# Kernel tuning notes

Measured on AMD Instinct MI355X. Metric: run time of the kernel, lower is better.

Reference implementation:

```python
import jax, jax.numpy as jnp
import numpy as np

N_NODES = 50000
N_EDGES = 800000
D_FEAT = 128
EMBED = 128
HEADS = 8
HEAD_DIM = EMBED // HEADS


def setup_inputs() -> dict:
    key = jax.random.key(0)
    ks = jax.random.split(key, 10)
    xavier = jax.nn.initializers.xavier_normal()
    return {
        "nodes": jax.random.normal(ks[0], (N_NODES, D_FEAT), jnp.float32),
        "edges": jax.random.normal(ks[1], (N_EDGES, D_FEAT), jnp.float32),
        "senders": jax.random.randint(ks[2], (N_EDGES,), 0, N_NODES, jnp.int32),
        "receivers": jax.random.randint(ks[3], (N_EDGES,), 0, N_NODES, jnp.int32),
        "Ws_k": xavier(ks[4], (D_FEAT, EMBED), jnp.float32),
        "Ws_b": jnp.zeros((EMBED,), jnp.float32),
        "Wr_k": xavier(ks[5], (D_FEAT, EMBED), jnp.float32),
        "Wr_b": jnp.zeros((EMBED,), jnp.float32),
        "We_k": xavier(ks[6], (D_FEAT, EMBED), jnp.float32),
        "We_b": jnp.zeros((EMBED,), jnp.float32),
        "a": xavier(ks[7], (HEADS, HEAD_DIM), jnp.float32),
    }


def reference(nodes, edges, senders, receivers, Ws_k, Ws_b, Wr_k, Wr_b, We_k, We_b, a):
    N = nodes.shape[0]
    E = edges.shape[0]
    H, D = a.shape
    # Node-level projections (linear, so equivalent to projecting gathered edge endpoints)
    hs = nodes @ Ws_k + Ws_b            # [N, HD]  (W_s on sent attributes)
    hr = nodes @ Wr_k + Wr_b            # [N, HD]  (W_r on received attributes)
    he = edges @ We_k + We_b            # [E, HD]  (W_e on edge attributes)
    sent = hs[senders]                  # [E, HD]
    x = jax.nn.leaky_relu(sent + hr[receivers] + he)  # default slope 0.01, as original
    xh = x.reshape(E, H, D)
    logits = jnp.sum(xh * a, axis=-1)   # [E, H]
    # segment_softmax over receivers (stable: subtract per-segment max)
    mx = jax.ops.segment_max(logits, receivers, num_segments=N)  # [N, H]
    mx = jnp.where(jnp.isfinite(mx), mx, 0.0)
    ex = jnp.exp(logits - mx[receivers])                         # [E, H]
    denom = jax.ops.segment_sum(ex, receivers, num_segments=N)   # [N, H]
    w = ex / denom[receivers]                                    # [E, H]
    msg = (w[..., None] * sent.reshape(E, H, D)).reshape(E, H * D)
    out = jax.ops.segment_sum(msg, receivers, num_segments=N)    # [N, HD]
    return out
```

## Files before the change

### kernel.cpp

```cpp
#include <hip/hip_runtime.h>

#define N_NODES 50000
#define N_EDGES 800000
#define D 128
#define HEADS 8

typedef __attribute__((ext_vector_type(8))) short short8b;
typedef __attribute__((ext_vector_type(4))) float f32x4;

__device__ __forceinline__ unsigned short f2bf_rne(float f) {
    unsigned int u = __float_as_uint(f);
    u += 0x7FFFu + ((u >> 16) & 1u);
    return (unsigned short)(u >> 16);
}
__device__ __forceinline__ float bf2f(unsigned short u) {
    return __uint_as_float(((unsigned int)u) << 16);
}

template <int CTRL>
__device__ __forceinline__ float dpp_radd(float v) {
    int s = __builtin_amdgcn_update_dpp(0, __float_as_int(v), CTRL, 0xF, 0xF, true);
    return v + __int_as_float(s);
}
__device__ __forceinline__ float rowsum16(float v) {
    v = dpp_radd<0xB1>(v);
    v = dpp_radd<0x4E>(v);
    v = dpp_radd<0x141>(v);
    v = dpp_radd<0x140>(v);
    return v;
}

#define K1_ROWS 128
__global__ __launch_bounds__(256, 3) void k_node_proj_mfma(
    const float* __restrict__ nodes,
    const float* __restrict__ Ws, const float* __restrict__ bs,
    const float* __restrict__ Wr, const float* __restrict__ br,
    unsigned short* __restrict__ hsb, unsigned short* __restrict__ hrb)
{
    __shared__ __align__(16) unsigned short WT[D][136];
    __shared__ __align__(16) unsigned short At[64][136];
    const int ntiles = (N_NODES + K1_ROWS - 1) / K1_ROWS;
    int bx = blockIdx.x;
    int proj = (bx >= ntiles) ? 1 : 0;
    int tile = proj ? (bx - ntiles) : bx;
    const float* W    = proj ? Wr : Ws;
    const float* bias = proj ? br : bs;
    unsigned short* outp = proj ? hrb : hsb;
    int t = threadIdx.x;
    int lane = t & 63;
    int wv = t >> 6;
    int lg = lane >> 4;
    int li = lane & 15;

    #pragma unroll 8
    for (int j = 0; j < 64; ++j) {
        int idx = t + 256 * j;
        int k = idx >> 7, c = idx & 127;
        WT[c][k] = f2bf_rne(W[idx]);
    }
    float b_ct[8];
    #pragma unroll
    for (int ct = 0; ct < 8; ++ct) b_ct[ct] = bias[ct * 16 + li];

    #pragma unroll 1
    for (int sub = 0; sub < 2; ++sub) {
        int row0 = tile * K1_ROWS + sub * 64;
        if (row0 >= N_NODES) break;
        __syncthreads();
        {
            const float4* Nv = (const float4*)nodes;
            #pragma unroll
            for (int j = 0; j < 8; ++j) {
                int fi = t + 256 * j;
                int r = row0 + (fi >> 5);
                float4 v = make_float4(0.f, 0.f, 0.f, 0.f);
                if (r < N_NODES) v = Nv[(size_t)r * 32 + (fi & 31)];
                ushort4 b;
                b.x = f2bf_rne(v.x); b.y = f2bf_rne(v.y);
                b.z = f2bf_rne(v.z); b.w = f2bf_rne(v.w);
                *(ushort4*)&At[fi >> 5][(fi & 31) * 4] = b;
            }
        }
        __syncthreads();

        short8b afr[4];
        #pragma unroll
        for (int kb = 0; kb < 4; ++kb)
            afr[kb] = *(const short8b*)&At[wv * 16 + li][kb * 32 + lg * 8];

        #pragma unroll
        for (int ct = 0; ct < 8; ++ct) {
            f32x4 acc = {0.f, 0.f, 0.f, 0.f};
            #pragma unroll
            for (int kb = 0; kb < 4; ++kb) {
                short8b bfr = *(const short8b*)&WT[ct * 16 + li][kb * 32 + lg * 8];
                acc = __builtin_amdgcn_mfma_f32_16x16x32_bf16(afr[kb], bfr, acc, 0, 0, 0);
            }
            #pragma unroll
            for (int j = 0; j < 4; ++j) {
                int r = row0 + wv * 16 + lg * 4 + j;
                if (r < N_NODES)
                    outp[(size_t)r * D + ct * 16 + li] = f2bf_rne(acc[j] + b_ct[ct]);
            }
        }
    }
}

__global__ __launch_bounds__(256) void k_hist(
    const int* __restrict__ receivers, int* __restrict__ deg)
{
    int i = blockIdx.x * 256 + threadIdx.x;
    if (i < N_EDGES) atomicAdd(&deg[receivers[i]], 1);
}

#define SCAN_CHUNK 49
__global__ __launch_bounds__(1024) void k_scan(
    const int* __restrict__ deg, int* __restrict__ rowptr, int* __restrict__ cursor)
{
    __shared__ int sm[1024];
    int t = threadIdx.x;
    int base = t * SCAN_CHUNK;
    int lsum = 0;
    #pragma unroll 4
    for (int i = 0; i < SCAN_CHUNK; ++i) {
        int idx = base + i;
        if (idx < N_NODES) lsum += deg[idx];
    }
    sm[t] = lsum;
    __syncthreads();
    for (int off = 1; off < 1024; off <<= 1) {
        int v = (t >= off) ? sm[t - off] : 0;
        __syncthreads();
        sm[t] += v;
        __syncthreads();
    }
    int run = (t > 0) ? sm[t - 1] : 0;
    for (int i = 0; i < SCAN_CHUNK; ++i) {
        int idx = base + i;
        if (idx < N_NODES) {
            rowptr[idx] = run;
            cursor[idx] = run;
            run += deg[idx];
        }
    }
    if (t == 1023) rowptr[N_NODES] = sm[1023];
}

__global__ __launch_bounds__(256) void k_fill(
    const int* __restrict__ receivers, const int* __restrict__ senders,
    int* __restrict__ cursor,
    int* __restrict__ s_csr, int* __restrict__ pos_csr)
{
    int i = blockIdx.x * 256 + threadIdx.x;
    if (i < N_EDGES) {
        int r = receivers[i];
        int pos = atomicAdd(&cursor[r], 1);
        s_csr[pos]  = senders[i];
        pos_csr[i]  = pos;
    }
}

#define BLK_E 64
__global__ __launch_bounds__(256, 3) void k_edge_logits_mfma(
    const float* __restrict__ edges,
    const int* __restrict__ senders, const int* __restrict__ receivers,
    const int* __restrict__ pos_csr,
    const float* __restrict__ We, const float* __restrict__ be,
    const float* __restrict__ a,
    const unsigned short* __restrict__ hsb, const unsigned short* __restrict__ hrb,
    float* __restrict__ ex)
{
    __shared__ __align__(16) unsigned short WeT[D][136];
    __shared__ __align__(16) unsigned short Et[BLK_E][136];
    int t = threadIdx.x;
    int lane = t & 63;
    int wv = t >> 6;
    int lg = lane >> 4;
    int li = lane & 15;

    #pragma unroll 8
    for (int j = 0; j < 64; ++j) {
        int idx = t + 256 * j;
        int k = idx >> 7, c = idx & 127;
        WeT[c][k] = f2bf_rne(We[idx]);
    }
    float a_h[HEADS], be_h[HEADS];
    #pragma unroll
    for (int h = 0; h < HEADS; ++h) {
        a_h[h]  = a[h * 16 + li];
        be_h[h] = be[h * 16 + li];
    }
    __syncthreads();

    const int ntiles = N_EDGES / BLK_E;
    const float4* Ev = (const float4*)edges;

    for (int tile = blockIdx.x; tile < ntiles; tile += gridDim.x) {
        int pb = tile * BLK_E + wv * 16;

        #pragma unroll
        for (int j = 0; j < 8; ++j) {
            int fi = lane + 64 * j;
            int rloc = fi >> 5;
            float4 v = Ev[(size_t)(pb + rloc) * 32 + (fi & 31)];
            ushort4 b;
            b.x = f2bf_rne(v.x); b.y = f2bf_rne(v.y);
            b.z = f2bf_rne(v.z); b.w = f2bf_rne(v.w);
            *(ushort4*)&Et[wv * 16 + rloc][(fi & 31) * 4] = b;
        }

        int sj[4], rj[4];
        #pragma unroll
        for (int j = 0; j < 4; ++j) {
            sj[j] = senders[pb + lg * 4 + j];
            rj[j] = receivers[pb + lg * 4 + j];
        }
        int o = 4 * lg + (li >> 2);
        int mypos = pos_csr[pb + o];

        unsigned short g_hs[4][HEADS], g_hr[4][HEADS];
        #pragma unroll
        for (int j = 0; j < 4; ++j) {
            const unsigned short* hsrow = hsb + (size_t)sj[j] * D + li;
            const unsigned short* hrrow = hrb + (size_t)rj[j] * D + li;
            #pragma unroll
            for (int h = 0; h < HEADS; ++h) {
                g_hs[j][h] = hsrow[h * 16];
                g_hr[j][h] = hrrow[h * 16];
            }
        }

        asm volatile("s_waitcnt lgkmcnt(0)" ::: "memory");
        __builtin_amdgcn_sched_barrier(0);

        short8b afr[4];
        #pragma unroll
        for (int kb = 0; kb < 4; ++kb)
            afr[kb] = *(const short8b*)&Et[wv * 16 + li][kb * 32 + lg * 8];

        float hold[8];
        #pragma unroll
        for (int h = 0; h < HEADS; ++h) {
            f32x4 acc = {0.f, 0.f, 0.f, 0.f};
            #pragma unroll
            for (int kb = 0; kb < 4; ++kb) {
                short8b bfr = *(const short8b*)&WeT[h * 16 + li][kb * 32 + lg * 8];
                acc = __builtin_amdgcn_mfma_f32_16x16x32_bf16(afr[kb], bfr, acc, 0, 0, 0);
            }
            float pr[4];
            #pragma unroll
            for (int j = 0; j < 4; ++j) {
                float x = acc[j] + be_h[h] + bf2f(g_hs[j][h]) + bf2f(g_hr[j][h]);
                x = fmaxf(x, 0.01f * x);
                pr[j] = rowsum16(x * a_h[h]);
            }
            float qa = (li & 4) ? pr[1] : pr[0];
            float qb = (li & 4) ? pr[3] : pr[2];
            hold[h] = __expf((li & 8) ? qb : qa);
        }
        {
            float a0 = (li & 1) ? hold[2] : hold[0];
            float a1 = (li & 1) ? hold[6] : hold[4];
            float ea = (li & 2) ? a1 : a0;
            float b0 = (li & 1) ? hold[3] : hold[1];
            float b1 = (li & 1) ? hold[7] : hold[5];
            float eb = (li & 2) ? b1 : b0;
            int h1 = 2 * (li & 3);
            *(float2*)&ex[(size_t)mypos * HEADS + h1] = make_float2(ea, eb);
        }
        __builtin_amdgcn_wave_barrier();
    }
}

__global__ __launch_bounds__(256) void k_gather_out(
    const int* __restrict__ rowptr, const int* __restrict__ s_csr,
    const unsigned short* __restrict__ hsb, const float* __restrict__ ex,
    float* __restrict__ out)
{
    int r = blockIdx.x * 4 + (threadIdx.x >> 6);
    int l = threadIdx.x & 63;
    int h = l >> 3;
    int beg = rowptr[r], end = rowptr[r + 1];

    float2 acc = make_float2(0.f, 0.f);
    float dsum = 0.f;
    for (int j0 = beg; j0 < end; j0 += 16) {
        int cnt = end - j0;
        int s[16]; float w[16];
        #pragma unroll
        for (int q = 0; q < 16; ++q)
            if (q < cnt) { s[q] = s_csr[j0 + q]; w[q] = ex[(size_t)(j0 + q) * HEADS + h]; }
        #pragma unroll
        for (int q = 0; q < 16; ++q)
            if (q < cnt) {
                ushort2 hv = *(const ushort2*)&hsb[(size_t)s[q] * D + 2 * l];
                acc.x += w[q] * bf2f(hv.x);
                acc.y += w[q] * bf2f(hv.y);
                dsum  += w[q];
            }
    }
    float inv = (end > beg && dsum != 0.f) ? (1.0f / dsum) : 0.f;
    acc.x *= inv; acc.y *= inv;
    *(float2*)&out[(size_t)r * D + 2 * l] = acc;
}

extern "C" void kernel_launch(void* const* d_in, const int* in_sizes, int n_in,
                              void* d_out, int out_size, void* d_ws, size_t ws_size,
                              hipStream_t stream) {
    const float* nodes     = (const float*)d_in[0];
    const float* edges     = (const float*)d_in[1];
    const int*   senders   = (const int*)d_in[2];
    const int*   receivers = (const int*)d_in[3];
    const float* Ws = (const float*)d_in[4];
    const float* bs = (const float*)d_in[5];
    const float* Wr = (const float*)d_in[6];
    const float* br = (const float*)d_in[7];
    const float* We = (const float*)d_in[8];
    const float* be = (const float*)d_in[9];
    const float* a  = (const float*)d_in[10];
    float* out = (float*)d_out;

    unsigned short* hsb = (unsigned short*)d_ws;
    unsigned short* hrb = hsb + (size_t)N_NODES * D;
    float* ex    = (float*)(hrb + (size_t)N_NODES * D);
    int* deg     = (int*)(ex + (size_t)N_EDGES * HEADS);
    int* rowptr  = deg + N_NODES;
    int* cursor  = rowptr + N_NODES + 1;
    int* s_csr   = cursor + N_NODES;
    int* pos_csr = s_csr + N_EDGES;

    (void)hipMemsetAsync(deg, 0, N_NODES * sizeof(int), stream);
    k_hist<<<N_EDGES / 256, 256, 0, stream>>>(receivers, deg);
    k_scan<<<1, 1024, 0, stream>>>(deg, rowptr, cursor);
    k_fill<<<N_EDGES / 256, 256, 0, stream>>>(receivers, senders, cursor,
                                              s_csr, pos_csr);
    int ntiles_n = (N_NODES + K1_ROWS - 1) / K1_ROWS;
    k_node_proj_mfma<<<ntiles_n * 2, 256, 0, stream>>>(nodes, Ws, bs, Wr, br, hsb, hrb);
    k_edge_logits_mfma<<<2500, 256, 0, stream>>>(edges, senders, receivers, pos_csr,
                                                 We, be, a, hsb, hrb, ex);
    k_gather_out<<<N_NODES / 4, 256, 0, stream>>>(rowptr, s_csr, hsb, ex, out);
}
```

Baseline: 444.1 us.

## Fuse node projections into histogram and CSR fill kernels

Splits the node projection kernel into its sender and receiver halves and merges each into a lightweight CSR-building kernel (histogram and fill) as extra blocks. The small, latency-bound atomic kernels then overlap with the compute-bound MFMA projection in the same launch, and one kernel launch disappears. In exchange, the atomic blocks inherit the projection kernel's launch bounds and its large static shared-memory footprint, which may cut how many of those blocks fit per CU.

Result: faster. 405.4 us, median of 2 (-8.7%).

```diff
diff --git a/kernel.cpp b/kernel.cpp
--- a/kernel.cpp
+++ b/kernel.cpp
@@ -31,21 +31,15 @@
 }
 
 #define K1_ROWS 128
-__global__ __launch_bounds__(256, 3) void k_node_proj_mfma(
-    const float* __restrict__ nodes,
-    const float* __restrict__ Ws, const float* __restrict__ bs,
-    const float* __restrict__ Wr, const float* __restrict__ br,
-    unsigned short* __restrict__ hsb, unsigned short* __restrict__ hrb)
+#define K1_TILES ((N_NODES + K1_ROWS - 1) / K1_ROWS)
+
+__device__ __forceinline__ void proj_body(
+    int tile, const float* __restrict__ nodes,
+    const float* __restrict__ W, const float* __restrict__ bias,
+    unsigned short* __restrict__ outp)
 {
     __shared__ __align__(16) unsigned short WT[D][136];
     __shared__ __align__(16) unsigned short At[64][136];
-    const int ntiles = (N_NODES + K1_ROWS - 1) / K1_ROWS;
-    int bx = blockIdx.x;
-    int proj = (bx >= ntiles) ? 1 : 0;
-    int tile = proj ? (bx - ntiles) : bx;
-    const float* W    = proj ? Wr : Ws;
-    const float* bias = proj ? br : bs;
-    unsigned short* outp = proj ? hrb : hsb;
     int t = threadIdx.x;
     int lane = t & 63;
     int wv = t >> 6;
@@ -106,11 +100,19 @@
     }
 }
 
-__global__ __launch_bounds__(256) void k_hist(
+__global__ __launch_bounds__(256, 3) void k_projS_hist(
+    const float* __restrict__ nodes,
+    const float* __restrict__ Ws, const float* __restrict__ bs,
+    unsigned short* __restrict__ hsb,
     const int* __restrict__ receivers, int* __restrict__ deg)
 {
-    int i = blockIdx.x * 256 + threadIdx.x;
-    if (i < N_EDGES) atomicAdd(&deg[receivers[i]], 1);
+    int bx = blockIdx.x;
+    if (bx < K1_TILES) {
+        proj_body(bx, nodes, Ws, bs, hsb);
+    } else {
+        int i = (bx - K1_TILES) * 256 + threadIdx.x;
+        if (i < N_EDGES) atomicAdd(&deg[receivers[i]], 1);
+    }
 }
 
 #define SCAN_CHUNK 49
@@ -146,17 +148,25 @@
     if (t == 1023) rowptr[N_NODES] = sm[1023];
 }
 
-__global__ __launch_bounds__(256) void k_fill(
+__global__ __launch_bounds__(256, 3) void k_projR_fill(
+    const float* __restrict__ nodes,
+    const float* __restrict__ Wr, const float* __restrict__ br,
+    unsigned short* __restrict__ hrb,
     const int* __restrict__ receivers, const int* __restrict__ senders,
     int* __restrict__ cursor,
     int* __restrict__ s_csr, int* __restrict__ pos_csr)
 {
-    int i = blockIdx.x * 256 + threadIdx.x;
-    if (i < N_EDGES) {
-        int r = receivers[i];
-        int pos = atomicAdd(&cursor[r], 1);
-        s_csr[pos]  = senders[i];
-        pos_csr[i]  = pos;
+    int bx = blockIdx.x;
+    if (bx < K1_TILES) {
+        proj_body(bx, nodes, Wr, br, hrb);
+    } else {
+        int i = (bx - K1_TILES) * 256 + threadIdx.x;
+        if (i < N_EDGES) {
+            int r = receivers[i];
+            int pos = atomicAdd(&cursor[r], 1);
+            s_csr[pos]  = senders[i];
+            pos_csr[i]  = pos;
+        }
     }
 }
 
@@ -329,13 +339,14 @@
     int* s_csr   = cursor + N_NODES;
     int* pos_csr = s_csr + N_EDGES;
 
+    const int HIST_BLKS = N_EDGES / 256;
+
     (void)hipMemsetAsync(deg, 0, N_NODES * sizeof(int), stream);
-    k_hist<<<N_EDGES / 256, 256, 0, stream>>>(receivers, deg);
+    k_projS_hist<<<K1_TILES + HIST_BLKS, 256, 0, stream>>>(
+        nodes, Ws, bs, hsb, receivers, deg);
     k_scan<<<1, 1024, 0, stream>>>(deg, rowptr, cursor);
-    k_fill<<<N_EDGES / 256, 256, 0, stream>>>(receivers, senders, cursor,
-                                              s_csr, pos_csr);
-    int ntiles_n = (N_NODES + K1_ROWS - 1) / K1_ROWS;
-    k_node_proj_mfma<<<ntiles_n * 2, 256, 0, stream>>>(nodes, Ws, bs, Wr, br, hsb, hrb);
+    k_projR_fill<<<K1_TILES + HIST_BLKS, 256, 0, stream>>>(
+        nodes, Wr, br, hrb, receivers, senders, cursor, s_csr, pos_csr);
     k_edge_logits_mfma<<<2500, 256, 0, stream>>>(edges, senders, receivers, pos_csr,
                                                  We, be, a, hsb, hrb, ex);
     k_gather_out<<<N_NODES / 4, 256, 0, stream>>>(rowptr, s_csr, hsb, ex, out);
```
